# Kernel optimization log

Measured on AMD Instinct MI355X. Metric: run time of the kernel, lower is better.

Reference implementation:

```python
import jax, jax.numpy as jnp
import numpy as np

EPS = 1e-12


def sage_pool_conv(x, src, dst, W_pool, b_pool, W_self, W_neigh, b, num_nodes):
    """DGL SAGEConv with aggregator_type='pool':
    h_neigh[v] = max_{u in N(v)} relu(x[u] @ W_pool + b_pool)
    out[v] = x[v] @ W_self + h_neigh[v] @ W_neigh + b
    Zero-in-degree nodes get h_neigh = 0 (DGL fills max over empty set with 0).
    """
    m = jax.nn.relu(x[src] @ W_pool + b_pool)            # [E, F] gathered + transformed
    agg = jax.ops.segment_max(m, dst, num_segments=num_nodes)  # [N, F], -inf where no neighbors
    agg = jnp.where(jnp.isneginf(agg), 0.0, agg)
    return x @ W_self + agg @ W_neigh + b


def l2norm_relu(h):
    # F.normalize(h, p=2, dim=1, eps=1e-12) then relu
    n = jnp.maximum(jnp.linalg.norm(h, axis=1, keepdims=True), EPS)
    return jax.nn.relu(h / n)


def setup_inputs() -> dict:
    key = jax.random.key(0)
    N, E = 50000, 1600000
    IN, HID, OUT = 128, 128, 128
    ks = jax.random.split(key, 16)
    s = 0.05
    return {
        "x": jax.random.normal(ks[0], (N, IN), dtype=jnp.float32),
        "src": jax.random.randint(ks[1], (E,), 0, N, dtype=jnp.int32),
        "dst": jax.random.randint(ks[2], (E,), 0, N, dtype=jnp.int32),
        "W_pool1": jax.random.normal(ks[3], (IN, IN), dtype=jnp.float32) * s,
        "b_pool1": jnp.zeros((IN,), dtype=jnp.float32),
        "W_self1": jax.random.normal(ks[4], (IN, HID), dtype=jnp.float32) * s,
        "W_neigh1": jax.random.normal(ks[5], (IN, HID), dtype=jnp.float32) * s,
        "b1": jnp.zeros((HID,), dtype=jnp.float32),
        "W_pool2": jax.random.normal(ks[6], (HID, HID), dtype=jnp.float32) * s,
        "b_pool2": jnp.zeros((HID,), dtype=jnp.float32),
        "W_self2": jax.random.normal(ks[7], (HID, OUT), dtype=jnp.float32) * s,
        "W_neigh2": jax.random.normal(ks[8], (HID, OUT), dtype=jnp.float32) * s,
        "b2": jnp.zeros((OUT,), dtype=jnp.float32),
    }


def reference(x, src, dst, W_pool1, b_pool1, W_self1, W_neigh1, b1,
              W_pool2, b_pool2, W_self2, W_neigh2, b2):
    N = x.shape[0]
    h = sage_pool_conv(x, src, dst, W_pool1, b_pool1, W_self1, W_neigh1, b1, N)
    h = l2norm_relu(h)
    # dropout_1 is re-assigned in the original forward but never applied -> no dropout
    h = sage_pool_conv(h, src, dst, W_pool2, b_pool2, W_self2, W_neigh2, b2, N)
    h = l2norm_relu(h)
    return h
```

## Files before the change

kernel.cpp:

```cpp
#include <hip/hip_runtime.h>
#include <hip/hip_bf16.h>

#define NF 128

typedef __attribute__((ext_vector_type(8))) short bf8;
typedef __attribute__((ext_vector_type(4))) float f4;

static __device__ __forceinline__ unsigned short f2bf(float f) {
  unsigned u = __builtin_bit_cast(unsigned, f);
  u = u + 0x7FFF + ((u >> 16) & 1);
  return (unsigned short)(u >> 16);
}


__global__ void k_convX(const float* __restrict__ A, unsigned short* __restrict__ B,
                        long long nelem, int* __restrict__ bcnt, int nb) {
  long long i = (long long)(blockIdx.x * blockDim.x + threadIdx.x) * 8;
  if (blockIdx.x == 0 && (int)threadIdx.x < nb) bcnt[threadIdx.x] = 0;
  if (i + 8 > nelem) return;
  float4 a = *(const float4*)(A + i);
  float4 b = *(const float4*)(A + i + 4);
  uint4 o;
  o.x = f2bf(a.x) | ((unsigned)f2bf(a.y) << 16);
  o.y = f2bf(a.z) | ((unsigned)f2bf(a.w) << 16);
  o.z = f2bf(b.x) | ((unsigned)f2bf(b.y) << 16);
  o.w = f2bf(b.z) | ((unsigned)f2bf(b.w) << 16);
  *(uint4*)(B + i) = o;
}


__global__ void k_packW(const float* W0, const float* W1, const float* W2,
                        const float* W3, const float* W4, const float* W5,
                        unsigned short* __restrict__ out) {
  int gid = blockIdx.x * blockDim.x + threadIdx.x;
  int m = gid >> 11;
  int u = gid & 2047;
  if (m >= 6) return;
  const float* W = (m == 0) ? W0 : (m == 1) ? W1 : (m == 2) ? W2
                 : (m == 3) ? W3 : (m == 4) ? W4 : W5;
  int l = u & 63, c = u >> 6;
  int kk = c & 3, t = c >> 2;
  int kb = kk * 32 + ((l >> 4) << 3);
  int n = t * 16 + (l & 15);
  unsigned short* o = out + (size_t)m * 2048 * 8 + (size_t)u * 8;
  #pragma unroll
  for (int j = 0; j < 8; ++j) o[j] = f2bf(W[(size_t)(kb + j) * NF + n]);
}


#define TILE_B 8192

__global__ __launch_bounds__(256) void k_bhist(const int* __restrict__ dst,
                                               int* __restrict__ bcnt, int E) {
  __shared__ int h[256];
  int tid = threadIdx.x;
  h[tid] = 0;
  __syncthreads();
  int t0 = blockIdx.x * TILE_B;
  int tend = min(E, t0 + TILE_B);
  for (int i = t0 + tid; i < tend; i += 256) atomicAdd(&h[dst[i] >> 8], 1);
  __syncthreads();
  if (h[tid] > 0) atomicAdd(&bcnt[tid], h[tid]);
}

__global__ __launch_bounds__(256) void k_bscan(const int* __restrict__ bcnt,
                                               int* __restrict__ boff,
                                               int* __restrict__ cursors,
                                               int* __restrict__ off,
                                               int nb, int N, int E) {
  __shared__ int sc[256];
  int tid = threadIdx.x;
  int v = (tid < nb) ? bcnt[tid] : 0;
  sc[tid] = v;
  __syncthreads();
  for (int d = 1; d < 256; d <<= 1) {
    int t = (tid >= d) ? sc[tid - d] : 0;
    __syncthreads();
    sc[tid] += t;
    __syncthreads();
  }
  if (tid < nb) {
    boff[tid + 1] = sc[tid];
    cursors[tid] = sc[tid] - v;
  }
  if (tid == 0) { boff[0] = 0; off[N] = E; }
}

__global__ __launch_bounds__(256) void k_binB(const int* __restrict__ src,
                                              const int* __restrict__ dst,
                                              int* __restrict__ cursors,
                                              unsigned* __restrict__ tmp, int E) {
  __shared__ int h[256], sc[256], gb[256], lc[256];
  __shared__ unsigned sorted[TILE_B];
  int tid = threadIdx.x;
  int t0 = blockIdx.x * TILE_B;
  int tcnt = min(E - t0, TILE_B);
  if (tcnt <= 0) return;
  h[tid] = 0;
  __syncthreads();
  for (int i = tid; i < tcnt; i += 256) atomicAdd(&h[dst[t0 + i] >> 8], 1);
  __syncthreads();
  int v = h[tid];
  sc[tid] = v;
  __syncthreads();
  for (int d = 1; d < 256; d <<= 1) {
    int t = (tid >= d) ? sc[tid - d] : 0;
    __syncthreads();
    sc[tid] += t;
    __syncthreads();
  }
  lc[tid] = 0;
  gb[tid] = (v > 0) ? atomicAdd(&cursors[tid], v) : 0;
  __syncthreads();
  for (int i = tid; i < tcnt; i += 256) {
    int d = dst[t0 + i];
    unsigned s = (unsigned)src[t0 + i];
    int b = d >> 8;
    int p = (sc[b] - h[b]) + atomicAdd(&lc[b], 1);
    sorted[p] = ((unsigned)b << 24) | (s << 8) | (unsigned)(d & 255);
  }
  __syncthreads();
  for (int i = tid; i < tcnt; i += 256) {
    unsigned ev = sorted[i];
    int b = ev >> 24;
    tmp[gb[b] + (i - (sc[b] - h[b]))] = ev & 0xFFFFFFu;
  }
}

#define CSR_CAP 15360

__global__ __launch_bounds__(256) void k_binC(const unsigned* __restrict__ tmp,
                                              const int* __restrict__ boff,
                                              int* __restrict__ off,
                                              int* __restrict__ esrc, int N) {
  __shared__ int lh[256], ls[256], lcur[256];
  __shared__ int csr[CSR_CAP];
  int tid = threadIdx.x;
  int b = blockIdx.x;
  int base = b << 8;
  int beg = boff[b], end = boff[b + 1];
  int cnt = end - beg;
  lh[tid] = 0;
  __syncthreads();
  for (int i = beg + tid; i < end; i += 256) atomicAdd(&lh[tmp[i] & 255], 1);
  __syncthreads();
  int v = lh[tid];
  ls[tid] = v;
  __syncthreads();
  for (int d = 1; d < 256; d <<= 1) {
    int t = (tid >= d) ? ls[tid - d] : 0;
    __syncthreads();
    ls[tid] += t;
    __syncthreads();
  }
  int excl = ls[tid] - v;
  if (base + tid < N) off[base + tid] = beg + excl;
  lcur[tid] = 0;
  __syncthreads();
  if (cnt <= CSR_CAP) {
    for (int i = beg + tid; i < end; i += 256) {
      unsigned e = tmp[i];
      int dl = (int)(e & 255);
      int p = (ls[dl] - lh[dl]) + atomicAdd(&lcur[dl], 1);
      csr[p] = (int)(e >> 8);
    }
    __syncthreads();
    for (int i = tid; i < cnt; i += 256) esrc[beg + i] = csr[i];
  } else {
    for (int i = beg + tid; i < end; i += 256) {
      unsigned e = tmp[i];
      int dl = (int)(e & 255);
      int p = (ls[dl] - lh[dl]) + atomicAdd(&lcur[dl], 1);
      esrc[beg + p] = (int)(e >> 8);
    }
  }
}


template <int NMAT, int OUT_MODE>
__global__ __launch_bounds__(256) void k_gemm(
    const unsigned short* __restrict__ A0, const unsigned short* __restrict__ P0,
    const unsigned short* __restrict__ A1, const unsigned short* __restrict__ P1,
    const float* __restrict__ bias, void* __restrict__ Cout, int M) {
  __shared__ __align__(16) char smem[NMAT * 32768];
  int tid = threadIdx.x, w = tid >> 6, lane = tid & 63;
  int r0 = lane & 15, g = lane >> 4;
  int base = blockIdx.x * 64;
  int rowbase = base + w * 16;
  int arow = min(rowbase + r0, M - 1);

  {
    uint4* S = (uint4*)smem;
    const uint4* Pv0 = (const uint4*)P0;
    for (int t = tid; t < 2048; t += 256) S[t] = Pv0[t];
    if (NMAT == 2) {
      const uint4* Pv1 = (const uint4*)P1;
      for (int t = tid; t < 2048; t += 256) S[2048 + t] = Pv1[t];
    }
  }
  __syncthreads();

  f4 acc[8];
  #pragma unroll
  for (int t = 0; t < 8; ++t) acc[t] = (f4){0.f, 0.f, 0.f, 0.f};

  #pragma unroll
  for (int mat = 0; mat < NMAT; ++mat) {
    const unsigned short* A = (mat == 0) ? A0 : A1;
    const bf8* Ar = (const bf8*)(A + (size_t)arow * NF);
    const bf8* Wl = (const bf8*)smem + (size_t)mat * 2048;
    #pragma unroll
    for (int kk = 0; kk < 4; ++kk) {
      bf8 a = Ar[kk * 4 + g];
      #pragma unroll
      for (int t = 0; t < 8; ++t) {
        bf8 b = Wl[(t * 4 + kk) * 64 + lane];
        acc[t] = __builtin_amdgcn_mfma_f32_16x16x32_bf16(a, b, acc[t], 0, 0, 0);
      }
    }
  }

  float bb[8];
  #pragma unroll
  for (int t = 0; t < 8; ++t) bb[t] = bias[t * 16 + r0];

  float val[8][4];
  #pragma unroll
  for (int t = 0; t < 8; ++t)
    #pragma unroll
    for (int i = 0; i < 4; ++i) val[t][i] = acc[t][i] + bb[t];

  float inv[4] = {1.f, 1.f, 1.f, 1.f};
  if (OUT_MODE != 0) {
    float ss[4] = {0.f, 0.f, 0.f, 0.f};
    #pragma unroll
    for (int i = 0; i < 4; ++i)
      #pragma unroll
      for (int t = 0; t < 8; ++t) ss[i] += val[t][i] * val[t][i];
    #pragma unroll
    for (int d = 1; d < 16; d <<= 1)
      #pragma unroll
      for (int i = 0; i < 4; ++i) ss[i] += __shfl_xor(ss[i], d, 64);
    #pragma unroll
    for (int i = 0; i < 4; ++i) inv[i] = 1.f / fmaxf(sqrtf(ss[i]), 1e-12f);
  }

  __syncthreads();
  int maxrows = min(64, M - base);

  if (OUT_MODE == 2) {
    float* So = (float*)smem;
    #pragma unroll
    for (int i = 0; i < 4; ++i)
      #pragma unroll
      for (int t = 0; t < 8; ++t)
        So[(w * 16 + g * 4 + i) * NF + t * 16 + r0] = fmaxf(val[t][i] * inv[i], 0.f);
    __syncthreads();
    uint4* Og = (uint4*)((float*)Cout + (size_t)base * NF);
    const uint4* Sv = (const uint4*)smem;
    int maxc = maxrows * 32;
    for (int c = tid; c < 2048; c += 256)
      if (c < maxc) Og[c] = Sv[c];
  } else {
    unsigned short* So = (unsigned short*)smem;
    #pragma unroll
    for (int i = 0; i < 4; ++i)
      #pragma unroll
      for (int t = 0; t < 8; ++t)
        So[(w * 16 + g * 4 + i) * NF + t * 16 + r0] =
            f2bf(fmaxf(val[t][i] * inv[i], 0.f));
    __syncthreads();
    uint4* Og = (uint4*)((unsigned short*)Cout + (size_t)base * NF);
    const uint4* Sv = (const uint4*)smem;
    int maxc = maxrows * 16;
    for (int c = tid; c < 1024; c += 256)
      if (c < maxc) Og[c] = Sv[c];
  }
}


__global__ __launch_bounds__(256) void k_gather_max(
    const unsigned short* __restrict__ Y, const int* __restrict__ off,
    const int* __restrict__ esrc, unsigned short* __restrict__ AGG, int N) {
  int w = (blockIdx.x * 256 + threadIdx.x) >> 6;
  int lane = threadIdx.x & 63;
  if (w >= N) return;
  int s = __builtin_amdgcn_readfirstlane(off[w]);
  int e = __builtin_amdgcn_readfirstlane(off[w + 1]);
  float ax = 0.f, ay = 0.f;
  for (int basei = s; basei < e; basei += 64) {
    int cnt = min(64, e - basei);
    int idxv = esrc[basei + min(lane, cnt - 1)];
    int i = 0;
    for (; i + 8 <= cnt; i += 8) {
      unsigned v[8];
      #pragma unroll
      for (int j = 0; j < 8; ++j) {
        int u = __builtin_amdgcn_readlane(idxv, i + j);
        v[j] = *((const unsigned*)(Y + (size_t)u * NF) + lane);
      }
      #pragma unroll
      for (int j = 0; j < 8; ++j) {
        ax = fmaxf(ax, __builtin_bit_cast(float, v[j] << 16));
        ay = fmaxf(ay, __builtin_bit_cast(float, v[j] & 0xFFFF0000u));
      }
    }
    for (; i < cnt; ++i) {
      int u = __builtin_amdgcn_readlane(idxv, i);
      unsigned v = *((const unsigned*)(Y + (size_t)u * NF) + lane);
      ax = fmaxf(ax, __builtin_bit_cast(float, v << 16));
      ay = fmaxf(ay, __builtin_bit_cast(float, v & 0xFFFF0000u));
    }
  }
  unsigned o = (unsigned)f2bf(ax) | ((unsigned)f2bf(ay) << 16);
  *(unsigned*)(AGG + (size_t)w * NF + lane * 2) = o;
}


extern "C" void kernel_launch(void* const* d_in, const int* in_sizes, int n_in,
                              void* d_out, int out_size, void* d_ws, size_t ws_size,
                              hipStream_t stream) {
  const float* x   = (const float*)d_in[0];
  const int*   src = (const int*)d_in[1];
  const int*   dst = (const int*)d_in[2];
  const float* Wp1 = (const float*)d_in[3];
  const float* bp1 = (const float*)d_in[4];
  const float* Ws1 = (const float*)d_in[5];
  const float* Wn1 = (const float*)d_in[6];
  const float* b1  = (const float*)d_in[7];
  const float* Wp2 = (const float*)d_in[8];
  const float* bp2 = (const float*)d_in[9];
  const float* Ws2 = (const float*)d_in[10];
  const float* Wn2 = (const float*)d_in[11];
  const float* b2  = (const float*)d_in[12];
  float* out = (float*)d_out;

  const int N = in_sizes[0] / NF;
  const int E = in_sizes[1];
  const int NB = (N + 255) >> 8;

  char* ws = (char*)d_ws;
  auto carve = [&](size_t bytes) { char* p = ws; ws += (bytes + 255) & ~(size_t)255; return p; };
  unsigned short* Xb    = (unsigned short*)carve((size_t)N * NF * 2);
  unsigned short* Yb    = (unsigned short*)carve((size_t)N * NF * 2);
  unsigned short* AGGb  = (unsigned short*)carve((size_t)N * NF * 2);
  unsigned short* Hb    = (unsigned short*)carve((size_t)N * NF * 2);
  unsigned short* Wpack = (unsigned short*)carve((size_t)6 * NF * NF * 2);
  int* off     = (int*)carve((size_t)(N + 1) * 4);
  int* bcnt    = (int*)carve((size_t)NB * 4);
  int* boff    = (int*)carve((size_t)(NB + 1) * 4);
  int* cursors = (int*)carve((size_t)NB * 4);
  unsigned* tmp = (unsigned*)carve((size_t)E * 4);
  int* esrc    = (int*)carve((size_t)E * 4);

  unsigned short* Pp1 = Wpack + 0 * NF * NF;
  unsigned short* Ps1 = Wpack + 1 * NF * NF;
  unsigned short* Pn1 = Wpack + 2 * NF * NF;
  unsigned short* Pp2 = Wpack + 3 * NF * NF;
  unsigned short* Ps2 = Wpack + 4 * NF * NF;
  unsigned short* Pn2 = Wpack + 5 * NF * NF;

  const long long nelX = (long long)N * NF;
  const int gConv = (int)((nelX / 8 + 255) / 256);
  const int gPack = (6 * 2048 + 255) / 256;
  const int gTile = (E + TILE_B - 1) / TILE_B;
  const int gG    = (N + 63) / 64;
  const int gRW   = (N + 3) / 4;

  k_convX<<<gConv, 256, 0, stream>>>(x, Xb, nelX, bcnt, NB);
  k_packW<<<gPack, 256, 0, stream>>>(Wp1, Ws1, Wn1, Wp2, Ws2, Wn2, Wpack);

  k_bhist<<<gTile, 256, 0, stream>>>(dst, bcnt, E);
  k_bscan<<<1, 256, 0, stream>>>(bcnt, boff, cursors, off, NB, N, E);
  k_binB<<<gTile, 256, 0, stream>>>(src, dst, cursors, tmp, E);
  k_binC<<<NB, 256, 0, stream>>>(tmp, boff, off, esrc, N);

  k_gemm<1, 0><<<gG, 256, 0, stream>>>(Xb, Pp1, nullptr, nullptr, bp1, Yb, N);
  k_gather_max<<<gRW, 256, 0, stream>>>(Yb, off, esrc, AGGb, N);
  k_gemm<2, 1><<<gG, 256, 0, stream>>>(Xb, Ps1, AGGb, Pn1, b1, Hb, N);

  k_gemm<1, 0><<<gG, 256, 0, stream>>>(Hb, Pp2, nullptr, nullptr, bp2, Yb, N);
  k_gather_max<<<gRW, 256, 0, stream>>>(Yb, off, esrc, AGGb, N);
  k_gemm<2, 2><<<gG, 256, 0, stream>>>(Hb, Ps2, AGGb, Pn2, b2, out, N);
}
```

Measured before the change: 302.6 us.

## Fuse neighbor max-gather into self/neigh GEMM and shrink edge indices

Merges the gather-max aggregation into the combined self/neighbor GEMM kernel. Aggregated rows are kept in shared memory instead of being written to and re-read from a global AGG buffer. The gather now has each lane load 16 bytes and process four edges per wave step, using packed u16 max on bf16 bits (valid because all values are post-ReLU and nonnegative) plus a cross-group shuffle reduction. Edge source indices are stored as 16-bit, which relies on N fitting in 16 bits; 50000 does, but a larger graph would not. The fused kernel reads weights straight from global memory rather than staging them in LDS, and runs the gather with only 64-node blocks, which may lower occupancy or load balance.

```diff
diff --git a/kernel.cpp b/kernel.cpp
--- a/kernel.cpp
+++ b/kernel.cpp
@@ -5,11 +5,28 @@
 
 typedef __attribute__((ext_vector_type(8))) short bf8;
 typedef __attribute__((ext_vector_type(4))) float f4;
+typedef unsigned short u16x8 __attribute__((ext_vector_type(8)));
 
 static __device__ __forceinline__ unsigned short f2bf(float f) {
   unsigned u = __builtin_bit_cast(unsigned, f);
   u = u + 0x7FFF + ((u >> 16) & 1);
   return (unsigned short)(u >> 16);
+}
+
+static __device__ __forceinline__ uint4 pkmax4(uint4 a, uint4 b) {
+  u16x8 x = __builtin_bit_cast(u16x8, a);
+  u16x8 y = __builtin_bit_cast(u16x8, b);
+  u16x8 m = __builtin_elementwise_max(x, y);
+  return __builtin_bit_cast(uint4, m);
+}
+
+static __device__ __forceinline__ uint4 shflxor4(uint4 a, int m) {
+  uint4 r;
+  r.x = (unsigned)__shfl_xor((int)a.x, m, 64);
+  r.y = (unsigned)__shfl_xor((int)a.y, m, 64);
+  r.z = (unsigned)__shfl_xor((int)a.z, m, 64);
+  r.w = (unsigned)__shfl_xor((int)a.w, m, 64);
+  return r;
 }
 
 
@@ -132,7 +149,7 @@
 __global__ __launch_bounds__(256) void k_binC(const unsigned* __restrict__ tmp,
                                               const int* __restrict__ boff,
                                               int* __restrict__ off,
-                                              int* __restrict__ esrc, int N) {
+                                              unsigned short* __restrict__ esrc, int N) {
   __shared__ int lh[256], ls[256], lcur[256];
   __shared__ int csr[CSR_CAP];
   int tid = threadIdx.x;
@@ -165,59 +182,133 @@
       csr[p] = (int)(e >> 8);
     }
     __syncthreads();
-    for (int i = tid; i < cnt; i += 256) esrc[beg + i] = csr[i];
+    for (int i = tid; i < cnt; i += 256) esrc[beg + i] = (unsigned short)csr[i];
   } else {
     for (int i = beg + tid; i < end; i += 256) {
       unsigned e = tmp[i];
       int dl = (int)(e & 255);
       int p = (ls[dl] - lh[dl]) + atomicAdd(&lcur[dl], 1);
-      esrc[beg + p] = (int)(e >> 8);
+      esrc[beg + p] = (unsigned short)(e >> 8);
     }
   }
 }
 
 
-template <int NMAT, int OUT_MODE>
-__global__ __launch_bounds__(256) void k_gemm(
-    const unsigned short* __restrict__ A0, const unsigned short* __restrict__ P0,
-    const unsigned short* __restrict__ A1, const unsigned short* __restrict__ P1,
-    const float* __restrict__ bias, void* __restrict__ Cout, int M) {
-  __shared__ __align__(16) char smem[NMAT * 32768];
+__global__ __launch_bounds__(256) void k_gemm_pool(
+    const unsigned short* __restrict__ A, const unsigned short* __restrict__ P,
+    const float* __restrict__ bias, unsigned short* __restrict__ Yout, int M) {
+  __shared__ __align__(16) char smem[32768];
   int tid = threadIdx.x, w = tid >> 6, lane = tid & 63;
   int r0 = lane & 15, g = lane >> 4;
   int base = blockIdx.x * 64;
-  int rowbase = base + w * 16;
-  int arow = min(rowbase + r0, M - 1);
+  int arow = min(base + w * 16 + r0, M - 1);
 
   {
     uint4* S = (uint4*)smem;
-    const uint4* Pv0 = (const uint4*)P0;
-    for (int t = tid; t < 2048; t += 256) S[t] = Pv0[t];
-    if (NMAT == 2) {
-      const uint4* Pv1 = (const uint4*)P1;
-      for (int t = tid; t < 2048; t += 256) S[2048 + t] = Pv1[t];
+    const uint4* Pv = (const uint4*)P;
+    for (int t = tid; t < 2048; t += 256) S[t] = Pv[t];
+  }
+  __syncthreads();
+
+  f4 acc[8];
+  #pragma unroll
+  for (int t = 0; t < 8; ++t) acc[t] = (f4){0.f, 0.f, 0.f, 0.f};
+
+  const bf8* Ar = (const bf8*)(A + (size_t)arow * NF);
+  const bf8* Wl = (const bf8*)smem;
+  #pragma unroll
+  for (int kk = 0; kk < 4; ++kk) {
+    bf8 a = Ar[kk * 4 + g];
+    #pragma unroll
+    for (int t = 0; t < 8; ++t) {
+      bf8 b = Wl[(t * 4 + kk) * 64 + lane];
+      acc[t] = __builtin_amdgcn_mfma_f32_16x16x32_bf16(a, b, acc[t], 0, 0, 0);
     }
   }
-  __syncthreads();
-
+
+  float bb[8];
+  #pragma unroll
+  for (int t = 0; t < 8; ++t) bb[t] = bias[t * 16 + r0];
+
+  __syncthreads();
+  unsigned short* So = (unsigned short*)smem;
+  #pragma unroll
+  for (int i = 0; i < 4; ++i)
+    #pragma unroll
+    for (int t = 0; t < 8; ++t)
+      So[(w * 16 + g * 4 + i) * NF + t * 16 + r0] = f2bf(fmaxf(acc[t][i] + bb[t], 0.f));
+  __syncthreads();
+  int maxrows = min(64, M - base);
+  uint4* Og = (uint4*)(Yout + (size_t)base * NF);
+  const uint4* Sv = (const uint4*)smem;
+  int maxc = maxrows * 16;
+  for (int c = tid; c < 1024; c += 256)
+    if (c < maxc) Og[c] = Sv[c];
+}
+
+
+template <int OUT_MODE>
+__global__ __launch_bounds__(256) void k_fused(
+    const unsigned short* __restrict__ Y, const int* __restrict__ off,
+    const unsigned short* __restrict__ esrc,
+    const unsigned short* __restrict__ X,
+    const unsigned short* __restrict__ Pself, const unsigned short* __restrict__ Pneigh,
+    const float* __restrict__ bias, void* __restrict__ Cout, int M) {
+  constexpr int SMEM = (OUT_MODE == 2) ? 32768 : 17408;
+  __shared__ __align__(16) char smem[SMEM];
+  unsigned short (*agg)[136] = (unsigned short (*)[136])smem;
+
+  int tid = threadIdx.x, w = tid >> 6, lane = tid & 63;
+  int r0 = lane & 15, g = lane >> 4;
+  int base = blockIdx.x * 64;
+
+  for (int n = 0; n < 16; ++n) {
+    int node = base + w * 16 + n;
+    uint4 am = {0u, 0u, 0u, 0u};
+    if (node < M) {
+      int s = __builtin_amdgcn_readfirstlane(off[node]);
+      int e = __builtin_amdgcn_readfirstlane(off[node + 1]);
+      for (int b0 = s; b0 < e; b0 += 64) {
+        int cnt = min(64, e - b0);
+        int idxv = (int)esrc[b0 + min(lane, cnt - 1)];
+        for (int i = 0; i < cnt; i += 16) {
+          #pragma unroll
+          for (int j = 0; j < 4; ++j) {
+            int eo = min(i + j * 4 + g, cnt - 1);
+            int u = __shfl(idxv, eo, 64);
+            uint4 v = *((const uint4*)(Y + (size_t)u * NF) + r0);
+            am = pkmax4(am, v);
+          }
+        }
+      }
+      am = pkmax4(am, shflxor4(am, 16));
+      am = pkmax4(am, shflxor4(am, 32));
+    }
+    if (g == 0) *(uint4*)&agg[w * 16 + n][r0 * 8] = am;
+  }
+  __syncthreads();
+
+  int arow = min(base + w * 16 + r0, M - 1);
   f4 acc[8];
   #pragma unroll
   for (int t = 0; t < 8; ++t) acc[t] = (f4){0.f, 0.f, 0.f, 0.f};
 
-  #pragma unroll
-  for (int mat = 0; mat < NMAT; ++mat) {
-    const unsigned short* A = (mat == 0) ? A0 : A1;
-    const bf8* Ar = (const bf8*)(A + (size_t)arow * NF);
-    const bf8* Wl = (const bf8*)smem + (size_t)mat * 2048;
-    #pragma unroll
-    for (int kk = 0; kk < 4; ++kk) {
-      bf8 a = Ar[kk * 4 + g];
-      #pragma unroll
-      for (int t = 0; t < 8; ++t) {
-        bf8 b = Wl[(t * 4 + kk) * 64 + lane];
-        acc[t] = __builtin_amdgcn_mfma_f32_16x16x32_bf16(a, b, acc[t], 0, 0, 0);
-      }
-    }
+  const bf8* Ar = (const bf8*)(X + (size_t)arow * NF);
+  const bf8* Bs = (const bf8*)Pself;
+  #pragma unroll
+  for (int kk = 0; kk < 4; ++kk) {
+    bf8 a = Ar[kk * 4 + g];
+    #pragma unroll
+    for (int t = 0; t < 8; ++t)
+      acc[t] = __builtin_amdgcn_mfma_f32_16x16x32_bf16(a, Bs[(t * 4 + kk) * 64 + lane], acc[t], 0, 0, 0);
+  }
+  const bf8* Bn = (const bf8*)Pneigh;
+  #pragma unroll
+  for (int kk = 0; kk < 4; ++kk) {
+    bf8 a = *(const bf8*)&agg[w * 16 + r0][kk * 32 + g * 8];
+    #pragma unroll
+    for (int t = 0; t < 8; ++t)
+      acc[t] = __builtin_amdgcn_mfma_f32_16x16x32_bf16(a, Bn[(t * 4 + kk) * 64 + lane], acc[t], 0, 0, 0);
   }
 
   float bb[8];
@@ -230,20 +321,18 @@
     #pragma unroll
     for (int i = 0; i < 4; ++i) val[t][i] = acc[t][i] + bb[t];
 
-  float inv[4] = {1.f, 1.f, 1.f, 1.f};
-  if (OUT_MODE != 0) {
-    float ss[4] = {0.f, 0.f, 0.f, 0.f};
-    #pragma unroll
-    for (int i = 0; i < 4; ++i)
-      #pragma unroll
-      for (int t = 0; t < 8; ++t) ss[i] += val[t][i] * val[t][i];
-    #pragma unroll
-    for (int d = 1; d < 16; d <<= 1)
-      #pragma unroll
-      for (int i = 0; i < 4; ++i) ss[i] += __shfl_xor(ss[i], d, 64);
-    #pragma unroll
-    for (int i = 0; i < 4; ++i) inv[i] = 1.f / fmaxf(sqrtf(ss[i]), 1e-12f);
-  }
+  float ss[4] = {0.f, 0.f, 0.f, 0.f};
+  #pragma unroll
+  for (int i = 0; i < 4; ++i)
+    #pragma unroll
+    for (int t = 0; t < 8; ++t) ss[i] += val[t][i] * val[t][i];
+  #pragma unroll
+  for (int d = 1; d < 16; d <<= 1)
+    #pragma unroll
+    for (int i = 0; i < 4; ++i) ss[i] += __shfl_xor(ss[i], d, 64);
+  float inv[4];
+  #pragma unroll
+  for (int i = 0; i < 4; ++i) inv[i] = 1.f / fmaxf(sqrtf(ss[i]), 1e-12f);
 
   __syncthreads();
   int maxrows = min(64, M - base);
@@ -267,8 +356,7 @@
     for (int i = 0; i < 4; ++i)
       #pragma unroll
       for (int t = 0; t < 8; ++t)
-        So[(w * 16 + g * 4 + i) * NF + t * 16 + r0] =
-            f2bf(fmaxf(val[t][i] * inv[i], 0.f));
+        So[(w * 16 + g * 4 + i) * NF + t * 16 + r0] = f2bf(fmaxf(val[t][i] * inv[i], 0.f));
     __syncthreads();
     uint4* Og = (uint4*)((unsigned short*)Cout + (size_t)base * NF);
     const uint4* Sv = (const uint4*)smem;
@@ -276,44 +364,6 @@
     for (int c = tid; c < 1024; c += 256)
       if (c < maxc) Og[c] = Sv[c];
   }
-}
-
-
-__global__ __launch_bounds__(256) void k_gather_max(
-    const unsigned short* __restrict__ Y, const int* __restrict__ off,
-    const int* __restrict__ esrc, unsigned short* __restrict__ AGG, int N) {
-  int w = (blockIdx.x * 256 + threadIdx.x) >> 6;
-  int lane = threadIdx.x & 63;
-  if (w >= N) return;
-  int s = __builtin_amdgcn_readfirstlane(off[w]);
-  int e = __builtin_amdgcn_readfirstlane(off[w + 1]);
-  float ax = 0.f, ay = 0.f;
-  for (int basei = s; basei < e; basei += 64) {
-    int cnt = min(64, e - basei);
-    int idxv = esrc[basei + min(lane, cnt - 1)];
-    int i = 0;
-    for (; i + 8 <= cnt; i += 8) {
-      unsigned v[8];
-      #pragma unroll
-      for (int j = 0; j < 8; ++j) {
-        int u = __builtin_amdgcn_readlane(idxv, i + j);
-        v[j] = *((const unsigned*)(Y + (size_t)u * NF) + lane);
-      }
-      #pragma unroll
-      for (int j = 0; j < 8; ++j) {
-        ax = fmaxf(ax, __builtin_bit_cast(float, v[j] << 16));
-        ay = fmaxf(ay, __builtin_bit_cast(float, v[j] & 0xFFFF0000u));
-      }
-    }
-    for (; i < cnt; ++i) {
-      int u = __builtin_amdgcn_readlane(idxv, i);
-      unsigned v = *((const unsigned*)(Y + (size_t)u * NF) + lane);
-      ax = fmaxf(ax, __builtin_bit_cast(float, v << 16));
-      ay = fmaxf(ay, __builtin_bit_cast(float, v & 0xFFFF0000u));
-    }
-  }
-  unsigned o = (unsigned)f2bf(ax) | ((unsigned)f2bf(ay) << 16);
-  *(unsigned*)(AGG + (size_t)w * NF + lane * 2) = o;
 }
 
 
@@ -343,7 +393,6 @@
   auto carve = [&](size_t bytes) { char* p = ws; ws += (bytes + 255) & ~(size_t)255; return p; };
   unsigned short* Xb    = (unsigned short*)carve((size_t)N * NF * 2);
   unsigned short* Yb    = (unsigned short*)carve((size_t)N * NF * 2);
-  unsigned short* AGGb  = (unsigned short*)carve((size_t)N * NF * 2);
   unsigned short* Hb    = (unsigned short*)carve((size_t)N * NF * 2);
   unsigned short* Wpack = (unsigned short*)carve((size_t)6 * NF * NF * 2);
   int* off     = (int*)carve((size_t)(N + 1) * 4);
@@ -351,7 +400,7 @@
   int* boff    = (int*)carve((size_t)(NB + 1) * 4);
   int* cursors = (int*)carve((size_t)NB * 4);
   unsigned* tmp = (unsigned*)carve((size_t)E * 4);
-  int* esrc    = (int*)carve((size_t)E * 4);
+  unsigned short* esrc = (unsigned short*)carve((size_t)E * 2);
 
   unsigned short* Pp1 = Wpack + 0 * NF * NF;
   unsigned short* Ps1 = Wpack + 1 * NF * NF;
@@ -365,7 +414,6 @@
   const int gPack = (6 * 2048 + 255) / 256;
   const int gTile = (E + TILE_B - 1) / TILE_B;
   const int gG    = (N + 63) / 64;
-  const int gRW   = (N + 3) / 4;
 
   k_convX<<<gConv, 256, 0, stream>>>(x, Xb, nelX, bcnt, NB);
   k_packW<<<gPack, 256, 0, stream>>>(Wp1, Ws1, Wn1, Wp2, Ws2, Wn2, Wpack);
@@ -375,11 +423,9 @@
   k_binB<<<gTile, 256, 0, stream>>>(src, dst, cursors, tmp, E);
   k_binC<<<NB, 256, 0, stream>>>(tmp, boff, off, esrc, N);
 
-  k_gemm<1, 0><<<gG, 256, 0, stream>>>(Xb, Pp1, nullptr, nullptr, bp1, Yb, N);
-  k_gather_max<<<gRW, 256, 0, stream>>>(Yb, off, esrc, AGGb, N);
-  k_gemm<2, 1><<<gG, 256, 0, stream>>>(Xb, Ps1, AGGb, Pn1, b1, Hb, N);
-
-  k_gemm<1, 0><<<gG, 256, 0, stream>>>(Hb, Pp2, nullptr, nullptr, bp2, Yb, N);
-  k_gather_max<<<gRW, 256, 0, stream>>>(Yb, off, esrc, AGGb, N);
-  k_gemm<2, 2><<<gG, 256, 0, stream>>>(Hb, Ps2, AGGb, Pn2, b2, out, N);
-}
+  k_gemm_pool<<<gG, 256, 0, stream>>>(Xb, Pp1, bp1, Yb, N);
+  k_fused<1><<<gG, 256, 0, stream>>>(Yb, off, esrc, Xb, Ps1, Pn1, b1, Hb, N);
+
+  k_gemm_pool<<<gG, 256, 0, stream>>>(Hb, Pp2, bp2, Yb, N);
+  k_fused<2><<<gG, 256, 0, stream>>>(Yb, off, esrc, Hb, Ps2, Pn2, b2, out, N);
+}
```

Result: faster. 291.0 us (-3.9%).
